# Optimization experiments

Measured on AMD Instinct MI355X. Metric: run time of the kernel, lower is better.

The kernel has to match this reference:

```python
import jax, jax.numpy as jnp
import numpy as np
import math

EMBED_DIM = 96
NUM_HEADS = 4
HEAD_DIM = EMBED_DIM // NUM_HEADS
RANGE_SIZES = (7, 9, 11)
SCALE = math.sqrt(HEAD_DIM)


def setup_inputs() -> dict:
    key = jax.random.key(0)
    ks = jax.random.split(key, 10)
    B, C, H, W = 2, EMBED_DIM, 64, 64
    s = 1.0 / math.sqrt(C)
    x = jax.random.normal(ks[0], (B, C, H, W), dtype=jnp.float32)
    wq = jax.random.normal(ks[1], (C, C), dtype=jnp.float32) * s
    bq = jax.random.normal(ks[2], (C,), dtype=jnp.float32) * 0.01
    wk = jax.random.normal(ks[3], (C, C), dtype=jnp.float32) * s
    bk = jax.random.normal(ks[4], (C,), dtype=jnp.float32) * 0.01
    wv = jax.random.normal(ks[5], (C, C), dtype=jnp.float32) * s
    bv = jax.random.normal(ks[6], (C,), dtype=jnp.float32) * 0.01
    wo = jax.random.normal(ks[7], (C, C * len(RANGE_SIZES)), dtype=jnp.float32) * (1.0 / math.sqrt(C * len(RANGE_SIZES)))
    bo = jax.random.normal(ks[8], (C,), dtype=jnp.float32) * 0.01
    return {"x": x, "wq": wq, "bq": bq, "wk": wk, "bk": bk,
            "wv": wv, "bv": bv, "wo": wo, "bo": bo}


def _conv1x1(x, w, b):
    # x: (B,Cin,H,W), w: (Cout,Cin) -> (B,Cout,H,W)
    return jnp.einsum('oc,bchw->bohw', w, x) + b[None, :, None, None]


def _unfold_patches(t, k):
    # t: (B,n,d,H,W) -> (B,n,d,k*k,H*W), zero-padded local neighborhoods,
    # kernel offsets row-major to match torch F.unfold ordering.
    B, n, d, H, W = t.shape
    p = k // 2
    tp = jnp.pad(t, ((0, 0), (0, 0), (0, 0), (p, p), (p, p)))
    pats = jnp.stack([tp[..., i:i + H, j:j + W]
                      for i in range(k) for j in range(k)], axis=3)
    return pats.reshape(B, n, d, k * k, H * W)


def reference(x, wq, bq, wk, bk, wv, bv, wo, bo):
    B, C, H, W = x.shape
    n, d = NUM_HEADS, HEAD_DIM
    Q = _conv1x1(x, wq, bq).reshape(B, n, d, H, W)
    K = _conv1x1(x, wk, bk).reshape(B, n, d, H, W)
    V = _conv1x1(x, wv, bv).reshape(B, n, d, H, W)
    Q_flat = Q.reshape(B, n, d, H * W)
    outputs = []
    for k in RANGE_SIZES:
        Kp = _unfold_patches(K, k)  # (B,n,d,kk,HW)
        Vp = _unfold_patches(V, k)
        scores = jnp.einsum('bndh,bndrh->bnrh', Q_flat, Kp) / SCALE
        attn = jax.nn.softmax(scores, axis=2)
        outputs.append(jnp.einsum('bnrh,bndrh->bndh', attn, Vp))
    concat = jnp.concatenate(outputs, axis=2)  # (B,n,d*len(ranges),HW)
    concat = concat.reshape(B, n * d * len(RANGE_SIZES), H, W)
    return _conv1x1(concat, wo, bo)
```

## Files before the change

kernel.cpp:

```cpp
#include <hip/hip_runtime.h>
#include <hip/hip_fp16.h>


#define HW    4096
#define NH    4
#define D     24
#define CC    96
#define C3    288
#define BATCH 2

#define TS    8
#define HALO  5
#define SW    18
#define SPIX  324
#define PSTR  24
#define PBS   29

#define INV_SCALE 0.20412414523193151f

typedef unsigned short u16;
typedef _Float16 h2f __attribute__((ext_vector_type(2)));

__device__ __forceinline__ float fdot2h(unsigned int a, unsigned int b, float c) {
#if __has_builtin(__builtin_amdgcn_fdot2)
    return __builtin_amdgcn_fdot2(__builtin_bit_cast(h2f, a),
                                  __builtin_bit_cast(h2f, b), c, false);
#else
    float2 fa = __half22float2(__builtin_bit_cast(__half2, a));
    float2 fb = __half22float2(__builtin_bit_cast(__half2, b));
    return fmaf(fa.x, fb.x, fmaf(fa.y, fb.y, c));
#endif
}

__device__ __forceinline__ unsigned int packh2(float a, float b) {
    return __builtin_bit_cast(unsigned int, __floats2half2_rn(a, b));
}

__global__ void prep_w(const float* __restrict__ wo, unsigned int* __restrict__ wh) {
    int idx = blockIdx.x * 256 + threadIdx.x;
    if (idx < CC * (C3 / 2)) {
        int o  = idx / (C3 / 2);
        int c2 = idx - o * (C3 / 2);
        wh[idx] = packh2(wo[o * C3 + 2 * c2], wo[o * C3 + 2 * c2 + 1]);
    }
}

__global__ __launch_bounds__(256) void qkv_kernel(
    const float* __restrict__ x,
    const float* __restrict__ wq, const float* __restrict__ bq,
    const float* __restrict__ wk, const float* __restrict__ bk,
    const float* __restrict__ wv, const float* __restrict__ bv,
    u16* __restrict__ Qh, u16* __restrict__ Kh, u16* __restrict__ Vh)
{
    int t   = threadIdx.x;
    int mat = blockIdx.y;
    const float* w    = (mat == 0) ? wq : (mat == 1) ? wk : wv;
    const float* bias = (mat == 0) ? bq : (mat == 1) ? bk : bv;
    u16* dst          = (mat == 0) ? Qh : (mat == 1) ? Kh : Vh;

    int gp = blockIdx.x * 64 + (t & 63);
    int b  = gp >> 12;
    int p  = gp & 4095;
    int o0 = blockIdx.z * 48 + __builtin_amdgcn_readfirstlane(t >> 6) * 12;

    const float* xb = x + (size_t)b * CC * HW + p;

    float acc[12];
    #pragma unroll
    for (int j = 0; j < 12; ++j) acc[j] = bias[o0 + j];

    #pragma unroll
    for (int cb = 0; cb < 6; ++cb) {
        float xc[16];
        #pragma unroll
        for (int i = 0; i < 16; ++i)
            xc[i] = xb[(size_t)(cb * 16 + i) * HW];
        #pragma unroll
        for (int j = 0; j < 12; ++j) {
            const float* wr = w + (o0 + j) * CC + cb * 16;
            #pragma unroll
            for (int i = 0; i < 16; ++i) acc[j] = fmaf(wr[i], xc[i], acc[j]);
        }
    }

    unsigned int u[6];
    #pragma unroll
    for (int i = 0; i < 6; ++i) u[i] = packh2(acc[2 * i], acc[2 * i + 1]);
    uint2* dp = (uint2*)(dst + (size_t)gp * CC + o0);
    dp[0] = make_uint2(u[0], u[1]);
    dp[1] = make_uint2(u[2], u[3]);
    dp[2] = make_uint2(u[4], u[5]);
}

__global__ __launch_bounds__(512) void attn_kernel(
    const u16* __restrict__ Qh, const u16* __restrict__ Kh,
    const u16* __restrict__ Vh, u16* __restrict__ att)
{
    __shared__ __align__(16) char smem_raw[8 * 64 * PBS * 4];
    u16* Ks = (u16*)smem_raw;
    u16* Vs = Ks + SPIX * PSTR;
    float* Pb = (float*)smem_raw;

    int t    = threadIdx.x;
    int wvid = __builtin_amdgcn_readfirstlane(t >> 6);
    int lane = t & 63;
    int bh = blockIdx.z;
    int b  = bh >> 2, h = bh & 3;
    int x0 = blockIdx.x * TS, y0 = blockIdx.y * TS;

    if (t < SPIX) {
        int sp = t;
        int sy = sp / SW, sx = sp - sy * SW;
        int gy = y0 + sy - HALO, gx = x0 + sx - HALO;
        uint4 k0 = make_uint4(0,0,0,0), k1 = k0, k2 = k0;
        uint4 v0 = k0, v1 = k0, v2 = k0;
        if ((unsigned)gy < 64u && (unsigned)gx < 64u) {
            size_t base = ((size_t)(b * HW + gy * 64 + gx) * CC + h * D);
            const uint4* ksrc = (const uint4*)(Kh + base);
            const uint4* vsrc = (const uint4*)(Vh + base);
            k0 = ksrc[0]; k1 = ksrc[1]; k2 = ksrc[2];
            v0 = vsrc[0]; v1 = vsrc[1]; v2 = vsrc[2];
        }
        uint4* kd = (uint4*)(Ks + sp * PSTR);
        uint4* vd = (uint4*)(Vs + sp * PSTR);
        kd[0] = k0; kd[1] = k1; kd[2] = k2;
        vd[0] = v0; vd[1] = v1; vd[2] = v2;
    }
    __syncthreads();

    int ty = lane >> 3, tx = lane & 7;
    int gp = b * HW + (y0 + ty) * 64 + (x0 + tx);

    unsigned int q[12];
    {
        const uint4* qs = (const uint4*)(Qh + (size_t)gp * CC + h * D);
        uint4 a = qs[0], bb = qs[1], c = qs[2];
        q[0]=a.x;  q[1]=a.y;  q[2]=a.z;  q[3]=a.w;
        q[4]=bb.x; q[5]=bb.y; q[6]=bb.z; q[7]=bb.w;
        q[8]=c.x;  q[9]=c.y;  q[10]=c.z; q[11]=c.w;
    }

    float acc[D];
    #pragma unroll
    for (int j = 0; j < D; ++j) acc[j] = 0.f;
    float l  = 0.f;
    int   cp = (ty + HALO) * SW + (tx + HALO);

    auto visit = [&](int di, int dj) {
        int sp = cp + di * SW + dj;
        const uint4* kp = (const uint4*)(Ks + sp * PSTR);
        uint4 k0 = kp[0], k1 = kp[1], k2 = kp[2];
        unsigned int ku[12] = {k0.x,k0.y,k0.z,k0.w, k1.x,k1.y,k1.z,k1.w, k2.x,k2.y,k2.z,k2.w};
        float s = 0.f;
        #pragma unroll
        for (int i = 0; i < 12; ++i) s = fdot2h(ku[i], q[i], s);
        float pw = __expf(s * INV_SCALE);
        l += pw;
        const uint4* vp = (const uint4*)(Vs + sp * PSTR);
        uint4 v0 = vp[0], v1 = vp[1], v2 = vp[2];
        unsigned int vu[12] = {v0.x,v0.y,v0.z,v0.w, v1.x,v1.y,v1.z,v1.w, v2.x,v2.y,v2.z,v2.w};
        #pragma unroll
        for (int i = 0; i < 12; ++i) {
            float2 f = __half22float2(__builtin_bit_cast(__half2, vu[i]));
            acc[2*i]   = fmaf(pw, f.x, acc[2*i]);
            acc[2*i+1] = fmaf(pw, f.y, acc[2*i+1]);
        }
    };

    if (wvid == 0) {
        #pragma unroll
        for (int k = 0; k < 49; k += 4) visit(k / 7 - 3, k % 7 - 3);
    } else if (wvid == 1) {
        #pragma unroll
        for (int k = 1; k < 49; k += 4) visit(k / 7 - 3, k % 7 - 3);
    } else if (wvid == 2) {
        #pragma unroll
        for (int k = 2; k < 49; k += 4) visit(k / 7 - 3, k % 7 - 3);
    } else if (wvid == 3) {
        #pragma unroll
        for (int k = 3; k < 49; k += 4) visit(k / 7 - 3, k % 7 - 3);
    } else if (wvid == 4) {
        #pragma unroll
        for (int dj = -4; dj <= 4; ++dj) visit(-4, dj);
        #pragma unroll
        for (int di = -3; di <= 3; ++di) visit(di, -4);
    } else if (wvid == 5) {
        #pragma unroll
        for (int dj = -4; dj <= 4; ++dj) visit(4, dj);
        #pragma unroll
        for (int di = -3; di <= 3; ++di) visit(di, 4);
    } else if (wvid == 6) {
        #pragma unroll
        for (int dj = -5; dj <= 5; ++dj) visit(-5, dj);
        #pragma unroll
        for (int di = -4; di <= 4; ++di) visit(di, -5);
    } else {
        #pragma unroll
        for (int dj = -5; dj <= 5; ++dj) visit(5, dj);
        #pragma unroll
        for (int di = -4; di <= 4; ++di) visit(di, 5);
    }

    __syncthreads();
    {
        float* pp = Pb + (wvid * 64 + lane) * PBS;
        pp[0] = l;
        #pragma unroll
        for (int i = 0; i < D; ++i) pp[1 + i] = acc[i];
    }
    __syncthreads();

    if (wvid < 3) {
        int N = (wvid == 0) ? 4 : (wvid == 1) ? 6 : 8;
        float L = 0.f;
        float a[D];
        #pragma unroll
        for (int i = 0; i < D; ++i) a[i] = 0.f;
        for (int s = 0; s < N; ++s) {
            const float* pp = Pb + (s * 64 + lane) * PBS;
            L += pp[0];
            #pragma unroll
            for (int i = 0; i < D; ++i) a[i] += pp[1 + i];
        }
        float rl = 1.0f / L;
        unsigned int u[12];
        #pragma unroll
        for (int i = 0; i < 12; ++i)
            u[i] = packh2(a[2 * i] * rl, a[2 * i + 1] * rl);
        uint4* dp = (uint4*)(att + (size_t)gp * C3 + h * 72 + wvid * D);
        dp[0] = make_uint4(u[0], u[1], u[2],  u[3]);
        dp[1] = make_uint4(u[4], u[5], u[6],  u[7]);
        dp[2] = make_uint4(u[8], u[9], u[10], u[11]);
    }
}

#define K3_PAD 65
__global__ __launch_bounds__(256) void proj_kernel(
    const u16* __restrict__ att, const unsigned int* __restrict__ wh,
    const float* __restrict__ bo, float* __restrict__ out)
{
    __shared__ unsigned int ab[(C3 / 2) * K3_PAD];

    int t   = threadIdx.x;
    int gp0 = blockIdx.x * 64;

    const uint4* src = (const uint4*)(att + (size_t)gp0 * C3);
    #pragma unroll
    for (int k = 0; k < 9; ++k) {
        int u   = t + k * 256;
        uint4 v = src[u];
        int px  = u / 36;
        int c20 = (u - px * 36) * 4;
        ab[(c20    ) * K3_PAD + px] = v.x;
        ab[(c20 + 1) * K3_PAD + px] = v.y;
        ab[(c20 + 2) * K3_PAD + px] = v.z;
        ab[(c20 + 3) * K3_PAD + px] = v.w;
    }
    __syncthreads();

    int wvid = __builtin_amdgcn_readfirstlane(t >> 6);
    int o0   = blockIdx.y * 24 + wvid * 6;
    int px   = t & 63;
    int gp   = gp0 + px;
    int b    = gp >> 12, p = gp & 4095;

    float acc[6];
    #pragma unroll
    for (int j = 0; j < 6; ++j) acc[j] = bo[o0 + j];

    #pragma unroll
    for (int cb = 0; cb < 9; ++cb) {
        unsigned int xp[16];
        #pragma unroll
        for (int i = 0; i < 16; ++i) xp[i] = ab[(cb * 16 + i) * K3_PAD + px];
        #pragma unroll
        for (int j = 0; j < 6; ++j) {
            const unsigned int* wr = wh + (o0 + j) * (C3 / 2) + cb * 16;
            #pragma unroll
            for (int i = 0; i < 16; ++i) acc[j] = fdot2h(xp[i], wr[i], acc[j]);
        }
    }

    #pragma unroll
    for (int j = 0; j < 6; ++j)
        out[(size_t)(b * CC + o0 + j) * HW + p] = acc[j];
}

extern "C" void kernel_launch(void* const* d_in, const int* in_sizes, int n_in,
                              void* d_out, int out_size, void* d_ws, size_t ws_size,
                              hipStream_t stream)
{
    const float* x  = (const float*)d_in[0];
    const float* wq = (const float*)d_in[1];
    const float* bq = (const float*)d_in[2];
    const float* wk = (const float*)d_in[3];
    const float* bk = (const float*)d_in[4];
    const float* wv = (const float*)d_in[5];
    const float* bv = (const float*)d_in[6];
    const float* wo = (const float*)d_in[7];
    const float* bo = (const float*)d_in[8];
    float* out = (float*)d_out;

    const size_t NPIX = (size_t)BATCH * HW;
    char* ws = (char*)d_ws;
    u16* Qh  = (u16*)ws;
    u16* Kh  = Qh + NPIX * CC;
    u16* Vh  = Kh + NPIX * CC;
    u16* att = Vh + NPIX * CC;
    unsigned int* wh = (unsigned int*)(att + NPIX * C3);

    prep_w<<<dim3(54), 256, 0, stream>>>(wo, wh);

    qkv_kernel<<<dim3(128, 3, 2), 256, 0, stream>>>(x, wq, bq, wk, bk, wv, bv, Qh, Kh, Vh);

    attn_kernel<<<dim3(8, 8, 8), 512, 0, stream>>>(Qh, Kh, Vh, att);

    proj_kernel<<<dim3(128, 4), 256, 0, stream>>>(att, wh, bo, out);
}
```

Before: 127.7 us.

## Fuse all stages into one cooperative persistent kernel with grid syncs

```diff
diff --git a/kernel.cpp b/kernel.cpp
--- a/kernel.cpp
+++ b/kernel.cpp
@@ -1,5 +1,8 @@
 #include <hip/hip_runtime.h>
 #include <hip/hip_fp16.h>
+#include <hip/hip_cooperative_groups.h>
+
+namespace cg = cooperative_groups;
 
 
 #define HW    4096
@@ -14,7 +17,7 @@
 #define SW    18
 #define SPIX  324
 #define PSTR  24
-#define PBS   29
+#define PBS   25
 
 #define INV_SCALE 0.20412414523193151f
 
@@ -36,33 +39,27 @@
     return __builtin_bit_cast(unsigned int, __floats2half2_rn(a, b));
 }
 
-__global__ void prep_w(const float* __restrict__ wo, unsigned int* __restrict__ wh) {
-    int idx = blockIdx.x * 256 + threadIdx.x;
-    if (idx < CC * (C3 / 2)) {
-        int o  = idx / (C3 / 2);
-        int c2 = idx - o * (C3 / 2);
-        wh[idx] = packh2(wo[o * C3 + 2 * c2], wo[o * C3 + 2 * c2 + 1]);
-    }
-}
-
-__global__ __launch_bounds__(256) void qkv_kernel(
-    const float* __restrict__ x,
+
+__device__ __forceinline__ void qkv_wave_task(
+    int task, int lane, const float* __restrict__ x,
     const float* __restrict__ wq, const float* __restrict__ bq,
     const float* __restrict__ wk, const float* __restrict__ bk,
     const float* __restrict__ wv, const float* __restrict__ bv,
     u16* __restrict__ Qh, u16* __restrict__ Kh, u16* __restrict__ Vh)
 {
-    int t   = threadIdx.x;
-    int mat = blockIdx.y;
+    int tw  = task & 3;
+    int pxg = (task >> 2) & 127;
+    int zm  = task >> 9;
+    int mat = zm % 3;
+    int z   = zm / 3;
     const float* w    = (mat == 0) ? wq : (mat == 1) ? wk : wv;
     const float* bias = (mat == 0) ? bq : (mat == 1) ? bk : bv;
     u16* dst          = (mat == 0) ? Qh : (mat == 1) ? Kh : Vh;
 
-    int gp = blockIdx.x * 64 + (t & 63);
+    int gp = pxg * 64 + lane;
     int b  = gp >> 12;
     int p  = gp & 4095;
-    int o0 = blockIdx.z * 48 + __builtin_amdgcn_readfirstlane(t >> 6) * 12;
-
+    int o0 = z * 48 + tw * 12;
     const float* xb = x + (size_t)b * CC * HW + p;
 
     float acc[12];
@@ -92,21 +89,18 @@
     dp[2] = make_uint2(u[4], u[5]);
 }
 
-__global__ __launch_bounds__(512) void attn_kernel(
+__device__ __forceinline__ void attn_tile(
+    int tile, int t, int wvid, int lane, char* smem,
     const u16* __restrict__ Qh, const u16* __restrict__ Kh,
     const u16* __restrict__ Vh, u16* __restrict__ att)
 {
-    __shared__ __align__(16) char smem_raw[8 * 64 * PBS * 4];
-    u16* Ks = (u16*)smem_raw;
-    u16* Vs = Ks + SPIX * PSTR;
-    float* Pb = (float*)smem_raw;
-
-    int t    = threadIdx.x;
-    int wvid = __builtin_amdgcn_readfirstlane(t >> 6);
-    int lane = t & 63;
-    int bh = blockIdx.z;
+    u16*   Ks = (u16*)smem;
+    u16*   Vs = Ks + SPIX * PSTR;
+    float* Pb = (float*)smem;
+
+    int bh = tile >> 6;
     int b  = bh >> 2, h = bh & 3;
-    int x0 = blockIdx.x * TS, y0 = blockIdx.y * TS;
+    int x0 = (tile & 7) * TS, y0 = ((tile >> 3) & 7) * TS;
 
     if (t < SPIX) {
         int sp = t;
@@ -134,10 +128,10 @@
     unsigned int q[12];
     {
         const uint4* qs = (const uint4*)(Qh + (size_t)gp * CC + h * D);
-        uint4 a = qs[0], bb = qs[1], c = qs[2];
+        uint4 a = qs[0], bb = qs[1], cq = qs[2];
         q[0]=a.x;  q[1]=a.y;  q[2]=a.z;  q[3]=a.w;
         q[4]=bb.x; q[5]=bb.y; q[6]=bb.z; q[7]=bb.w;
-        q[8]=c.x;  q[9]=c.y;  q[10]=c.z; q[11]=c.w;
+        q[8]=cq.x; q[9]=cq.y; q[10]=cq.z; q[11]=cq.w;
     }
 
     float acc[D];
@@ -234,47 +228,41 @@
     }
 }
 
-#define K3_PAD 65
-__global__ __launch_bounds__(256) void proj_kernel(
+__device__ __forceinline__ void proj_group(
+    int grp, int t, int wvid, int lane, int nthreads, char* smem,
     const u16* __restrict__ att, const unsigned int* __restrict__ wh,
     const float* __restrict__ bo, float* __restrict__ out)
 {
-    __shared__ unsigned int ab[(C3 / 2) * K3_PAD];
-
-    int t   = threadIdx.x;
-    int gp0 = blockIdx.x * 64;
+    unsigned int* ab = (unsigned int*)smem;
+    int gp0 = grp * 64;
 
     const uint4* src = (const uint4*)(att + (size_t)gp0 * C3);
-    #pragma unroll
-    for (int k = 0; k < 9; ++k) {
-        int u   = t + k * 256;
-        uint4 v = src[u];
-        int px  = u / 36;
-        int c20 = (u - px * 36) * 4;
-        ab[(c20    ) * K3_PAD + px] = v.x;
-        ab[(c20 + 1) * K3_PAD + px] = v.y;
-        ab[(c20 + 2) * K3_PAD + px] = v.z;
-        ab[(c20 + 3) * K3_PAD + px] = v.w;
+    for (int u = t; u < 2304; u += nthreads) {
+        uint4 v  = src[u];
+        int px   = u / 36;
+        int c20  = (u - px * 36) * 4;
+        ab[(c20    ) * 65 + px] = v.x;
+        ab[(c20 + 1) * 65 + px] = v.y;
+        ab[(c20 + 2) * 65 + px] = v.z;
+        ab[(c20 + 3) * 65 + px] = v.w;
     }
     __syncthreads();
 
-    int wvid = __builtin_amdgcn_readfirstlane(t >> 6);
-    int o0   = blockIdx.y * 24 + wvid * 6;
-    int px   = t & 63;
-    int gp   = gp0 + px;
-    int b    = gp >> 12, p = gp & 4095;
-
-    float acc[6];
-    #pragma unroll
-    for (int j = 0; j < 6; ++j) acc[j] = bo[o0 + j];
+    int o0 = wvid * 12;
+    int gp = gp0 + lane;
+    int b  = gp >> 12, p = gp & 4095;
+
+    float acc[12];
+    #pragma unroll
+    for (int j = 0; j < 12; ++j) acc[j] = bo[o0 + j];
 
     #pragma unroll
     for (int cb = 0; cb < 9; ++cb) {
         unsigned int xp[16];
         #pragma unroll
-        for (int i = 0; i < 16; ++i) xp[i] = ab[(cb * 16 + i) * K3_PAD + px];
-        #pragma unroll
-        for (int j = 0; j < 6; ++j) {
+        for (int i = 0; i < 16; ++i) xp[i] = ab[(cb * 16 + i) * 65 + lane];
+        #pragma unroll
+        for (int j = 0; j < 12; ++j) {
             const unsigned int* wr = wh + (o0 + j) * (C3 / 2) + cb * 16;
             #pragma unroll
             for (int i = 0; i < 16; ++i) acc[j] = fdot2h(xp[i], wr[i], acc[j]);
@@ -282,9 +270,100 @@
     }
 
     #pragma unroll
-    for (int j = 0; j < 6; ++j)
+    for (int j = 0; j < 12; ++j)
         out[(size_t)(b * CC + o0 + j) * HW + p] = acc[j];
 }
+
+
+__global__ __launch_bounds__(512, 2) void fused_kernel(
+    const float* __restrict__ x,
+    const float* __restrict__ wq, const float* __restrict__ bq,
+    const float* __restrict__ wk, const float* __restrict__ bk,
+    const float* __restrict__ wv, const float* __restrict__ bv,
+    const float* __restrict__ wo, const float* __restrict__ bo,
+    u16* __restrict__ Qh, u16* __restrict__ Kh, u16* __restrict__ Vh,
+    u16* __restrict__ att, unsigned int* __restrict__ wh,
+    float* __restrict__ out)
+{
+    cg::grid_group grid = cg::this_grid();
+    __shared__ __align__(16) char smem[51200];
+
+    const int t    = threadIdx.x;
+    const int blk  = blockIdx.x;
+    const int wvid = __builtin_amdgcn_readfirstlane(t >> 6);
+    const int lane = t & 63;
+
+    {
+        int idx = blk * 512 + t;
+        if (idx < CC * (C3 / 2)) {
+            int o  = idx / (C3 / 2);
+            int c2 = idx - o * (C3 / 2);
+            wh[idx] = packh2(wo[o * C3 + 2 * c2], wo[o * C3 + 2 * c2 + 1]);
+        }
+    }
+
+    {
+        int wave_gid = blk * 8 + wvid;
+        for (int task = wave_gid; task < 3072; task += 2048)
+            qkv_wave_task(task, lane, x, wq, bq, wk, bk, wv, bv, Qh, Kh, Vh);
+    }
+
+    grid.sync();
+
+    #pragma unroll
+    for (int tt = 0; tt < 2; ++tt) {
+        attn_tile(blk * 2 + tt, t, wvid, lane, smem, Qh, Kh, Vh, att);
+        __syncthreads();
+    }
+
+    grid.sync();
+
+    if (blk < 128)
+        proj_group(blk, t, wvid, lane, 512, smem, att, wh, bo, out);
+}
+
+
+__global__ void prep_w(const float* __restrict__ wo, unsigned int* __restrict__ wh) {
+    int idx = blockIdx.x * 256 + threadIdx.x;
+    if (idx < CC * (C3 / 2)) {
+        int o  = idx / (C3 / 2);
+        int c2 = idx - o * (C3 / 2);
+        wh[idx] = packh2(wo[o * C3 + 2 * c2], wo[o * C3 + 2 * c2 + 1]);
+    }
+}
+
+__global__ __launch_bounds__(256) void qkv_kernel(
+    const float* __restrict__ x,
+    const float* __restrict__ wq, const float* __restrict__ bq,
+    const float* __restrict__ wk, const float* __restrict__ bk,
+    const float* __restrict__ wv, const float* __restrict__ bv,
+    u16* __restrict__ Qh, u16* __restrict__ Kh, u16* __restrict__ Vh)
+{
+    int t = threadIdx.x;
+    int task = (blockIdx.y * 128 + blockIdx.x) * 4 + (t >> 6);
+    qkv_wave_task(task, t & 63, x, wq, bq, wk, bk, wv, bv, Qh, Kh, Vh);
+}
+
+__global__ __launch_bounds__(512) void attn_kernel(
+    const u16* __restrict__ Qh, const u16* __restrict__ Kh,
+    const u16* __restrict__ Vh, u16* __restrict__ att)
+{
+    __shared__ __align__(16) char smem[51200];
+    int t = threadIdx.x;
+    attn_tile(blockIdx.x, t, __builtin_amdgcn_readfirstlane(t >> 6), t & 63,
+              smem, Qh, Kh, Vh, att);
+}
+
+__global__ __launch_bounds__(512) void proj_kernel(
+    const u16* __restrict__ att, const unsigned int* __restrict__ wh,
+    const float* __restrict__ bo, float* __restrict__ out)
+{
+    __shared__ __align__(16) char smem[37440];
+    int t = threadIdx.x;
+    proj_group(blockIdx.x, t, __builtin_amdgcn_readfirstlane(t >> 6), t & 63,
+               512, smem, att, wh, bo, out);
+}
+
 
 extern "C" void kernel_launch(void* const* d_in, const int* in_sizes, int n_in,
                               void* d_out, int out_size, void* d_ws, size_t ws_size,
@@ -309,11 +388,19 @@
     u16* att = Vh + NPIX * CC;
     unsigned int* wh = (unsigned int*)(att + NPIX * C3);
 
-    prep_w<<<dim3(54), 256, 0, stream>>>(wo, wh);
-
-    qkv_kernel<<<dim3(128, 3, 2), 256, 0, stream>>>(x, wq, bq, wk, bk, wv, bv, Qh, Kh, Vh);
-
-    attn_kernel<<<dim3(8, 8, 8), 512, 0, stream>>>(Qh, Kh, Vh, att);
-
-    proj_kernel<<<dim3(128, 4), 256, 0, stream>>>(att, wh, bo, out);
-}
+    void* args[] = {
+        (void*)&x, (void*)&wq, (void*)&bq, (void*)&wk, (void*)&bk,
+        (void*)&wv, (void*)&bv, (void*)&wo, (void*)&bo,
+        (void*)&Qh, (void*)&Kh, (void*)&Vh, (void*)&att, (void*)&wh,
+        (void*)&out
+    };
+    hipError_t err = hipLaunchCooperativeKernel((const void*)fused_kernel,
+                                                dim3(256), dim3(512), args, 0, stream);
+    if (err != hipSuccess) {
+        prep_w<<<dim3(54), 256, 0, stream>>>(wo, wh);
+        qkv_kernel<<<dim3(128, 6), 256, 0, stream>>>(x, wq, bq, wk, bk, wv, bv,
+                                                     Qh, Kh, Vh);
+        attn_kernel<<<dim3(512), 512, 0, stream>>>(Qh, Kh, Vh, att);
+        proj_kernel<<<dim3(128), 512, 0, stream>>>(att, wh, bo, out);
+    }
+}
```

Measured after the change: 242.8 us. +90.2%, slower.
